# Optimization experiments

Measured on AMD Instinct MI355X. Metric: run time of the kernel, lower is better.

## Reference

```python
import jax, jax.numpy as jnp
import numpy as np

F_DIM = 512
N_HEADS = 8
D_Q = 64
D_V = 64
EPS = 1e-6


def _xavier(key, shape):
    fan_in, fan_out = shape[0], shape[1]
    limit = float(np.sqrt(6.0 / (fan_in + fan_out)))
    return jax.random.uniform(key, shape, jnp.float32, -limit, limit)


def layer_norm(x, g, b):
    mu = jnp.mean(x, axis=-1, keepdims=True)
    var = jnp.mean(jnp.square(x - mu), axis=-1, keepdims=True)
    return (x - mu) * jax.lax.rsqrt(var + EPS) * g + b


def setup_inputs() -> dict:
    key = jax.random.key(0)
    ks = jax.random.split(key, 16)
    B, V, F = 4, 2048, F_DIM
    inp = {
        "texture_map1": jax.random.normal(ks[0], (B, V, F), jnp.float32),
        "texture_map2": jax.random.normal(ks[1], (B, V, F), jnp.float32),
        "ln1_g": jnp.ones((F,), jnp.float32), "ln1_b": jnp.zeros((F,), jnp.float32),
        "ln2_g": jnp.ones((F,), jnp.float32), "ln2_b": jnp.zeros((F,), jnp.float32),
        "Wq": _xavier(ks[2], (F, N_HEADS * D_Q)), "bq": jnp.zeros((N_HEADS * D_Q,), jnp.float32),
        "Wk": _xavier(ks[3], (F, N_HEADS * D_Q)), "bk": jnp.zeros((N_HEADS * D_Q,), jnp.float32),
        "Wv": _xavier(ks[4], (F, N_HEADS * D_V)), "bv": jnp.zeros((N_HEADS * D_V,), jnp.float32),
        "Wfc": _xavier(ks[5], (N_HEADS * D_V, F)), "bfc": jnp.zeros((F,), jnp.float32),
        "ff1_ln_g": jnp.ones((F,), jnp.float32), "ff1_ln_b": jnp.zeros((F,), jnp.float32),
        "ff1_W1": _xavier(ks[6], (F, F)), "ff1_b1": jnp.zeros((F,), jnp.float32),
        "ff1_W2": _xavier(ks[7], (F, F)), "ff1_b2": jnp.zeros((F,), jnp.float32),
        "ff2_ln_g": jnp.ones((F,), jnp.float32), "ff2_ln_b": jnp.zeros((F,), jnp.float32),
        "ff2_W1": _xavier(ks[8], (F, F)), "ff2_b1": jnp.zeros((F,), jnp.float32),
        "ff2_W2": _xavier(ks[9], (F, F)), "ff2_b2": jnp.zeros((F,), jnp.float32),
    }
    return inp


def _heads(x, d):
    B, V, _ = x.shape
    return x.reshape(B, V, N_HEADS, d).transpose(0, 2, 1, 3)  # [B,H,V,d]


def _ff_block(x, ln_g, ln_b, W1, b1, W2, b2):
    h = layer_norm(x, ln_g, ln_b)
    h = jax.nn.relu(h @ W1 + b1) @ W2 + b2
    return x + h


def reference(texture_map1, texture_map2, ln1_g, ln1_b, ln2_g, ln2_b,
              Wq, bq, Wk, bk, Wv, bv, Wfc, bfc,
              ff1_ln_g, ff1_ln_b, ff1_W1, ff1_b1, ff1_W2, ff1_b2,
              ff2_ln_g, ff2_ln_b, ff2_W1, ff2_b1, ff2_W2, ff2_b2):
    B, V, F = texture_map1.shape
    norm = D_Q ** 0.5
    t1n = layer_norm(texture_map1, ln1_g, ln1_b)
    t2n = layer_norm(texture_map2, ln2_g, ln2_b)
    q1 = _heads(t1n @ Wq + bq, D_Q)
    k1 = _heads(t1n @ Wk + bk, D_Q)
    v1 = _heads(t1n @ Wv + bv, D_V)
    q2 = _heads(t2n @ Wq + bq, D_Q)
    k2 = _heads(t2n @ Wk + bk, D_Q)
    v2 = _heads(t2n @ Wv + bv, D_V)
    # cross attention: 1 attends to 2, 2 attends to 1
    attn12 = jax.nn.softmax(jnp.einsum('bhqd,bhkd->bhqk', q1, k2) / norm, axis=-1)
    attn21 = jax.nn.softmax(jnp.einsum('bhqd,bhkd->bhqk', q2, k1) / norm, axis=-1)
    f12 = jnp.einsum('bhqk,bhkd->bhqd', attn12, v2).transpose(0, 2, 1, 3).reshape(B, V, -1)
    f21 = jnp.einsum('bhqk,bhkd->bhqd', attn21, v1).transpose(0, 2, 1, 3).reshape(B, V, -1)
    f12 = f12 @ Wfc + bfc
    f21 = f21 @ Wfc + bfc
    out1 = _ff_block(texture_map1 + f12, ff1_ln_g, ff1_ln_b, ff1_W1, ff1_b1, ff1_W2, ff1_b2)
    out2 = _ff_block(texture_map2 + f21, ff2_ln_g, ff2_ln_b, ff2_W1, ff2_b1, ff2_W2, ff2_b2)
    return (out1, out2)
```

## Files before the change

### kernel.cpp

```cpp
#include <hip/hip_runtime.h>
#include <stdint.h>

#define FD    512
#define SEQ   2048
#define NHALF 8192
#define NTOT  16384
#define QKVN  1536

typedef unsigned short u16;
typedef __attribute__((ext_vector_type(8))) short short8;
typedef __attribute__((ext_vector_type(4))) float f32x4;

__device__ __forceinline__ u16 f2bf(float f){
  union { float f; uint32_t i; } v; v.f = f;
  uint32_t r = v.i + 0x7FFFu + ((v.i >> 16) & 1u);
  return (u16)(r >> 16);
}

__device__ __forceinline__ void gload_lds16(const void* g, void* l){
  __builtin_amdgcn_global_load_lds((const __attribute__((address_space(1))) void*)g,
                                   (__attribute__((address_space(3))) void*)l, 16, 0, 0);
}

__device__ __forceinline__ f32x4 mfma16(short8 a, short8 b, f32x4 c){
  return __builtin_amdgcn_mfma_f32_16x16x32_bf16(a, b, c, 0, 0, 0);
}

__device__ __forceinline__ uint32_t cvtpk(float lo, float hi){
  uint32_t r; asm("v_cvt_pk_bf16_f32 %0, %1, %2" : "=v"(r) : "v"(lo), "v"(hi)); return r;
}

__device__ __forceinline__ float fexp2(float x){
  float r; asm("v_exp_f32 %0, %1" : "=v"(r) : "v"(x)); return r;
}

__global__ __launch_bounds__(256) void wconv_kernel(
    const float* __restrict__ w0, const float* __restrict__ w1,
    const float* __restrict__ w2, const float* __restrict__ w3,
    const float* __restrict__ w4, const float* __restrict__ w5,
    const float* __restrict__ w6, const float* __restrict__ w7,
    u16* __restrict__ out)
{
  int mat = blockIdx.x >> 6;
  const float* w = w0;
  switch (mat){ case 1: w=w1; break; case 2: w=w2; break; case 3: w=w3; break;
                case 4: w=w4; break; case 5: w=w5; break; case 6: w=w6; break;
                case 7: w=w7; break; default: break; }
  int tile = blockIdx.x & 63;
  int k0 = (tile >> 3) << 6, n0 = (tile & 7) << 6;

  __shared__ float lt[64][65];
  int tid = threadIdx.x;
  int tr = tid >> 4, tc = (tid & 15) << 2;
  #pragma unroll
  for (int p = 0; p < 4; p++){
    int k = p * 16 + tr;
    float4 v = *(const float4*)&w[(size_t)(k0 + k) * 512 + n0 + tc];
    lt[k][tc] = v.x; lt[k][tc + 1] = v.y; lt[k][tc + 2] = v.z; lt[k][tc + 3] = v.w;
  }
  __syncthreads();
  int n = tid >> 2, kc = (tid & 3) << 4;
  u16 buf[16];
  #pragma unroll
  for (int j = 0; j < 16; j++) buf[j] = f2bf(lt[kc + j][n]);
  u16* dst = out + ((size_t)mat << 18) + (size_t)(n0 + n) * 512 + k0 + kc;
  *(short8*)dst       = *(const short8*)(buf);
  *(short8*)(dst + 8) = *(const short8*)(buf + 8);
}

__global__ __launch_bounds__(256) void biascat_kernel(
    const float* __restrict__ bq, const float* __restrict__ bk,
    const float* __restrict__ bv, float* __restrict__ o)
{
  int i = blockIdx.x * 256 + threadIdx.x;
  if (i < 512) o[i] = bq[i];
  else if (i < 1024) o[i] = bk[i - 512];
  else o[i] = bv[i - 1024];
}

__global__ __launch_bounds__(256) void ln_kernel(
    const float* __restrict__ xa, const float* __restrict__ xb,
    const float* __restrict__ ga, const float* __restrict__ ba,
    const float* __restrict__ gb, const float* __restrict__ bb,
    u16* __restrict__ out)
{
  int row = blockIdx.x;
  const float* x; const float* g; const float* bi;
  if (row < NHALF){ x = xa + (size_t)row * FD; g = ga; bi = ba; }
  else            { x = xb + (size_t)(row - NHALF) * FD; g = gb; bi = bb; }
  int t = threadIdx.x;
  float2 v = ((const float2*)x)[t];
  __shared__ float red[8];
  float s = v.x + v.y;
  #pragma unroll
  for (int o = 32; o; o >>= 1) s += __shfl_xor(s, o, 64);
  if ((t & 63) == 0) red[t >> 6] = s;
  __syncthreads();
  float mu = (red[0] + red[1] + red[2] + red[3]) * (1.0f / 512.0f);
  float d0 = v.x - mu, d1 = v.y - mu;
  float q = d0 * d0 + d1 * d1;
  #pragma unroll
  for (int o = 32; o; o >>= 1) q += __shfl_xor(q, o, 64);
  if ((t & 63) == 0) red[4 + (t >> 6)] = q;
  __syncthreads();
  float var = (red[4] + red[5] + red[6] + red[7]) * (1.0f / 512.0f);
  float rs = rsqrtf(var + 1e-6f);
  out[(size_t)row * FD + 2 * t]     = f2bf(d0 * rs * g[2 * t]     + bi[2 * t]);
  out[(size_t)row * FD + 2 * t + 1] = f2bf(d1 * rs * g[2 * t + 1] + bi[2 * t + 1]);
}

__global__ __launch_bounds__(256) void vtr_kernel(
    const u16* __restrict__ qkv, u16* __restrict__ vt)
{
  int kc = blockIdx.x & 15;
  int s  = blockIdx.x >> 4;
  int dir = s >> 5, b = (s >> 3) & 3, h = s & 7;
  int t = threadIdx.x;
  int d = t & 63, kb = t >> 6;
  const u16* src = qkv + (size_t)(dir * NHALF + b * SEQ + kc * 128 + kb * 32) * QKVN
                       + 1024 + h * 64 + d;
  u16* dst = vt + (size_t)s * 131072 + (size_t)d * 2048 + kc * 128 + kb * 32;
  u16 buf[32];
  #pragma unroll
  for (int j = 0; j < 32; j++) buf[j] = src[(size_t)j * QKVN];
  #pragma unroll
  for (int j = 0; j < 4; j++)
    *(short8*)(dst + j * 8) = *(const short8*)(buf + j * 8);
}

template<bool RELU, bool OUT_BF16, bool HAS_RES>
__global__ __launch_bounds__(256) void gemm_bt(
    const u16* __restrict__ A,
    const u16* __restrict__ BtLo, const u16* __restrict__ BtHi,
    const float* __restrict__ biasLo, const float* __restrict__ biasHi,
    const float* __restrict__ resLo, const float* __restrict__ resHi,
    void* __restrict__ outp,
    int M, int N, int K, int halfM)
{
  __shared__ __align__(16) u16 lA[2][128 * 32];
  __shared__ __align__(16) u16 lB[2][128 * 32];
  int nwg = gridDim.x;
  int bid = (blockIdx.x & 7) * (nwg >> 3) + (blockIdx.x >> 3);
  int nTN = N >> 7;
  int bm = bid / nTN, bn = bid - bm * nTN;
  int rowBase = bm << 7, colBase = bn << 7;
  bool lo = rowBase < halfM;
  const u16* Bt = lo ? BtLo : BtHi;
  const float* bias = lo ? biasLo : biasHi;
  const float* res = lo ? resLo : resHi;
  int rowLocalBase = lo ? rowBase : rowBase - halfM;

  int tid = threadIdx.x, wv = tid >> 6, ln = tid & 63;

  f32x4 acc[4][4];
  #pragma unroll
  for (int m = 0; m < 4; m++)
    #pragma unroll
    for (int n = 0; n < 4; n++) acc[m][n] = (f32x4){0.f, 0.f, 0.f, 0.f};

  int off0 = tid * 16, off1 = 4096 + tid * 16;
  int r0 = off0 >> 6, c0 = (off0 & 63) >> 1;
  int r1 = off1 >> 6, c1 = (off1 & 63) >> 1;
  const u16* gA0 = A + (size_t)(rowBase + r0) * K + c0;
  const u16* gA1 = A + (size_t)(rowBase + r1) * K + c1;
  const u16* gB0 = Bt + (size_t)(colBase + r0) * K + c0;
  const u16* gB1 = Bt + (size_t)(colBase + r1) * K + c1;

  int arow = (wv >> 1) << 6, bcol = (wv & 1) << 6;

  #define STAGE(buf, kt) do { \
    gload_lds16(gA0 + (kt), (char*)lA[buf] + wv * 1024); \
    gload_lds16(gA1 + (kt), (char*)lA[buf] + 4096 + wv * 1024); \
    gload_lds16(gB0 + (kt), (char*)lB[buf] + wv * 1024); \
    gload_lds16(gB1 + (kt), (char*)lB[buf] + 4096 + wv * 1024); } while (0)

  STAGE(0, 0);
  __syncthreads();

  int nK = K >> 5;
  for (int i = 0; i < nK; i++){
    int cur = i & 1;
    if (i + 1 < nK) STAGE(cur ^ 1, (i + 1) << 5);
    short8 af[4], bfr[4];
    #pragma unroll
    for (int m = 0; m < 4; m++)
      af[m] = *(const short8*)&lA[cur][(arow + (m << 4) + (ln & 15)) * 32 + ((ln >> 4) << 3)];
    #pragma unroll
    for (int n = 0; n < 4; n++)
      bfr[n] = *(const short8*)&lB[cur][(bcol + (n << 4) + (ln & 15)) * 32 + ((ln >> 4) << 3)];
    #pragma unroll
    for (int m = 0; m < 4; m++)
      #pragma unroll
      for (int n = 0; n < 4; n++)
        acc[m][n] = mfma16(af[m], bfr[n], acc[m][n]);
    __syncthreads();
  }
  #undef STAGE

  #pragma unroll
  for (int n = 0; n < 4; n++){
    int col = colBase + bcol + (n << 4) + (ln & 15);
    float bv = bias[col];
    #pragma unroll
    for (int m = 0; m < 4; m++){
      int rowT = arow + (m << 4) + ((ln >> 4) << 2);
      #pragma unroll
      for (int r = 0; r < 4; r++){
        float v = acc[m][n][r] + bv;
        if (RELU) v = fmaxf(v, 0.f);
        if (HAS_RES) v += res[(size_t)(rowLocalBase + rowT + r) * N + col];
        if (OUT_BF16) ((u16*)outp)[(size_t)(rowBase + rowT + r) * N + col] = f2bf(v);
        else ((float*)outp)[(size_t)(rowBase + rowT + r) * N + col] = v;
      }
    }
  }
}

__global__ __launch_bounds__(512, 4) void attn_kernel(
    const u16* __restrict__ qkv, const u16* __restrict__ vt, u16* __restrict__ fb)
{
  int l = (blockIdx.x & 7) * 64 + (blockIdx.x >> 3);
  int qt = l & 7;
  int h  = (l >> 3) & 7;
  int z  = l >> 6;
  int dir = z >> 2, b = z & 3;
  int qRow0  = dir * NHALF + b * SEQ + qt * 256;
  int kvRow0 = (dir ^ 1) * NHALF + b * SEQ;
  int colQ = h * 64;

  __shared__ __align__(16) u16 lK[2][64 * 64];
  __shared__ __align__(16) u16 lVt[2][64 * 64];
  __shared__ __align__(16) u16 lP[8][32 * 64];

  int tid = threadIdx.x, wv = tid >> 6, ln = tid & 63;
  int g = ln >> 4, lo = ln & 15;

  int srow = tid >> 3;
  int soff = ((tid & 7) ^ (srow & 7)) * 8;

  const float CEXP = 0.18033688f;

  int ca0 = (g * 8) ^ ((lo & 7) << 3);
  int ca1 = (32 + g * 8) ^ ((lo & 7) << 3);
  int lo64 = lo * 64;

  int pidx[4];
  #pragma unroll
  for (int n = 0; n < 4; n++)
    pidx[n] = lo64 + ((n * 16 + g * 4) ^ ((lo & 7) << 3));
  int pra = lo64 + ca0, prb = lo64 + ca1;

  const u16* qbase  = qkv + (size_t)qRow0 * QKVN + colQ;
  const u16* vtbase = vt + (size_t)((dir ^ 1) * 32 + b * 8 + h) * 131072;

  const u16* kp0 = qkv + (size_t)(kvRow0 + srow) * QKVN + 512 + colQ + soff;
  const u16* vp0 = vtbase + (size_t)srow * 2048 + soff;

  char* dK0 = (char*)lK[0] + wv * 1024;
  char* dV0 = (char*)lVt[0] + wv * 1024;
  const u16* lKf = &lK[0][0];
  const u16* lVf = &lVt[0][0];
  u16* lPw = &lP[wv][0];

  gload_lds16(qbase + (size_t)srow * QKVN + soff,         (char*)lK[0]  + wv * 1024);
  gload_lds16(qbase + (size_t)(64 + srow) * QKVN + soff,  (char*)lK[1]  + wv * 1024);
  gload_lds16(qbase + (size_t)(128 + srow) * QKVN + soff, (char*)lVt[0] + wv * 1024);
  gload_lds16(qbase + (size_t)(192 + srow) * QKVN + soff, (char*)lVt[1] + wv * 1024);
  __syncthreads();
  const u16* qh;
  switch (wv >> 1){ case 0: qh = lK[0]; break; case 1: qh = lK[1]; break;
                    case 2: qh = lVt[0]; break; default: qh = lVt[1]; break; }
  int qr0 = (wv & 1) * 32 + lo;
  short8 qf00 = *(const short8*)&qh[qr0 * 64 + ca0];
  short8 qf01 = *(const short8*)&qh[qr0 * 64 + ca1];
  short8 qf10 = *(const short8*)&qh[(qr0 + 16) * 64 + ca0];
  short8 qf11 = *(const short8*)&qh[(qr0 + 16) * 64 + ca1];
  __syncthreads();

  gload_lds16(kp0, dK0);
  gload_lds16(vp0, dV0);
  kp0 += (size_t)64 * QKVN; vp0 += 64;
  __syncthreads();

  f32x4 acc_o0[4], acc_o1[4];
  #pragma unroll
  for (int nd = 0; nd < 4; nd++){
    acc_o0[nd] = (f32x4){0.f, 0.f, 0.f, 0.f};
    acc_o1[nd] = (f32x4){0.f, 0.f, 0.f, 0.f};
  }
  f32x4 acc_l0 = (f32x4){0.f, 0.f, 0.f, 0.f};
  f32x4 acc_l1 = (f32x4){0.f, 0.f, 0.f, 0.f};
  float m_l0, m_l1;
  const f32x4 z4 = (f32x4){0.f, 0.f, 0.f, 0.f};

  short8 ones;
  #pragma unroll
  for (int j = 0; j < 8; j++) ones[j] = (short)0x3F80;

  int cb = 0;
  for (int t = 0; t < 32; t++){
    if (t < 31){
      int nb = cb ^ 8192;
      gload_lds16(kp0, dK0 + nb);
      gload_lds16(vp0, dV0 + nb);
      kp0 += (size_t)64 * QKVN; vp0 += 64;
    }
    const u16* lk = (const u16*)((const char*)lKf + cb);
    const u16* lv = (const u16*)((const char*)lVf + cb);

    f32x4 s0[4], s1[4];
    #pragma unroll
    for (int n = 0; n < 4; n++){
      short8 kfa = *(const short8*)&lk[lo64 + n * 1024 + ca0];
      short8 kfb = *(const short8*)&lk[lo64 + n * 1024 + ca1];
      s0[n] = mfma16(kfa, qf00, z4);
      s0[n] = mfma16(kfb, qf01, s0[n]);
      s1[n] = mfma16(kfa, qf10, z4);
      s1[n] = mfma16(kfb, qf11, s1[n]);
    }

    float m00, m01;
    {
      float t0 = fmaxf(fmaxf(s0[0][0], s0[0][1]), fmaxf(s0[0][2], s0[0][3]));
      float t1 = fmaxf(fmaxf(s0[1][0], s0[1][1]), fmaxf(s0[1][2], s0[1][3]));
      float t2 = fmaxf(fmaxf(s0[2][0], s0[2][1]), fmaxf(s0[2][2], s0[2][3]));
      float t3 = fmaxf(fmaxf(s0[3][0], s0[3][1]), fmaxf(s0[3][2], s0[3][3]));
      m00 = fmaxf(fmaxf(t0, t1), fmaxf(t2, t3));
      m00 = fmaxf(m00, __shfl_xor(m00, 16, 64));
      m00 = fmaxf(m00, __shfl_xor(m00, 32, 64));
      m00 *= CEXP;
    }
    {
      float t0 = fmaxf(fmaxf(s1[0][0], s1[0][1]), fmaxf(s1[0][2], s1[0][3]));
      float t1 = fmaxf(fmaxf(s1[1][0], s1[1][1]), fmaxf(s1[1][2], s1[1][3]));
      float t2 = fmaxf(fmaxf(s1[2][0], s1[2][1]), fmaxf(s1[2][2], s1[2][3]));
      float t3 = fmaxf(fmaxf(s1[3][0], s1[3][1]), fmaxf(s1[3][2], s1[3][3]));
      m01 = fmaxf(fmaxf(t0, t1), fmaxf(t2, t3));
      m01 = fmaxf(m01, __shfl_xor(m01, 16, 64));
      m01 = fmaxf(m01, __shfl_xor(m01, 32, 64));
      m01 *= CEXP;
    }

    if (t == 0){ m_l0 = m00; m_l1 = m01; }

    #pragma unroll
    for (int n = 0; n < 4; n++){
      float p0 = fexp2(fmaf(s0[n][0], CEXP, -m_l0));
      float p1 = fexp2(fmaf(s0[n][1], CEXP, -m_l0));
      float p2 = fexp2(fmaf(s0[n][2], CEXP, -m_l0));
      float p3 = fexp2(fmaf(s0[n][3], CEXP, -m_l0));
      uint2 pk0; pk0.x = cvtpk(p0, p1); pk0.y = cvtpk(p2, p3);
      *(uint2*)&lPw[pidx[n]] = pk0;
      float q0 = fexp2(fmaf(s1[n][0], CEXP, -m_l1));
      float q1 = fexp2(fmaf(s1[n][1], CEXP, -m_l1));
      float q2 = fexp2(fmaf(s1[n][2], CEXP, -m_l1));
      float q3 = fexp2(fmaf(s1[n][3], CEXP, -m_l1));
      uint2 pk1; pk1.x = cvtpk(q0, q1); pk1.y = cvtpk(q2, q3);
      *(uint2*)&lPw[pidx[n] + 1024] = pk1;
    }

    short8 pf00 = *(const short8*)&lPw[pra];
    short8 pf01 = *(const short8*)&lPw[prb];
    short8 pf10 = *(const short8*)&lPw[pra + 1024];
    short8 pf11 = *(const short8*)&lPw[prb + 1024];
    acc_l0 = mfma16(pf00, ones, acc_l0);
    acc_l0 = mfma16(pf01, ones, acc_l0);
    acc_l1 = mfma16(pf10, ones, acc_l1);
    acc_l1 = mfma16(pf11, ones, acc_l1);
    #pragma unroll
    for (int nd = 0; nd < 4; nd++){
      short8 vfa = *(const short8*)&lv[lo64 + nd * 1024 + ca0];
      short8 vfb = *(const short8*)&lv[lo64 + nd * 1024 + ca1];
      acc_o0[nd] = mfma16(pf00, vfa, acc_o0[nd]);
      acc_o0[nd] = mfma16(pf01, vfb, acc_o0[nd]);
      acc_o1[nd] = mfma16(pf10, vfa, acc_o1[nd]);
      acc_o1[nd] = mfma16(pf11, vfb, acc_o1[nd]);
    }

    bool ok = (m00 <= m_l0 + 8.f) && (m01 <= m_l1 + 8.f);
    if (!__all(ok)){
      float mn0 = fmaxf(m_l0, m00);
      float mn1 = fmaxf(m_l1, m01);
      float a00 = fexp2(m_l0 - mn0);
      float a01 = fexp2(m_l1 - mn1);
      m_l0 = mn0; m_l1 = mn1;
      #pragma unroll
      for (int r = 0; r < 4; r++){
        float ar0 = __shfl(a00, g * 4 + r, 64);
        float ar1 = __shfl(a01, g * 4 + r, 64);
        acc_l0[r] *= ar0;
        acc_l1[r] *= ar1;
        #pragma unroll
        for (int nd = 0; nd < 4; nd++){
          acc_o0[nd][r] *= ar0;
          acc_o1[nd][r] *= ar1;
        }
      }
    }

    cb ^= 8192;
    __syncthreads();
  }

  #pragma unroll
  for (int r = 0; r < 4; r++){
    float rl0 = 1.0f / acc_l0[r];
    float rl1 = 1.0f / acc_l1[r];
    #pragma unroll
    for (int nd = 0; nd < 4; nd++){
      int row0 = qRow0 + wv * 32 + g * 4 + r;
      int d    = colQ + (nd << 4) + lo;
      fb[(size_t)row0 * FD + d]        = f2bf(acc_o0[nd][r] * rl0);
      fb[(size_t)(row0 + 16) * FD + d] = f2bf(acc_o1[nd][r] * rl1);
    }
  }
}

extern "C" void kernel_launch(void* const* d_in, const int* in_sizes, int n_in,
                              void* d_out, int out_size, void* d_ws, size_t ws_size,
                              hipStream_t stream)
{
  const float* t1   = (const float*)d_in[0];
  const float* t2   = (const float*)d_in[1];
  const float* ln1g = (const float*)d_in[2];
  const float* ln1b = (const float*)d_in[3];
  const float* ln2g = (const float*)d_in[4];
  const float* ln2b = (const float*)d_in[5];
  const float* Wq   = (const float*)d_in[6];
  const float* bq   = (const float*)d_in[7];
  const float* Wk   = (const float*)d_in[8];
  const float* bk   = (const float*)d_in[9];
  const float* Wv   = (const float*)d_in[10];
  const float* bv   = (const float*)d_in[11];
  const float* Wfc  = (const float*)d_in[12];
  const float* bfc  = (const float*)d_in[13];
  const float* f1lg = (const float*)d_in[14];
  const float* f1lb = (const float*)d_in[15];
  const float* W11  = (const float*)d_in[16];
  const float* b11  = (const float*)d_in[17];
  const float* W12  = (const float*)d_in[18];
  const float* b12  = (const float*)d_in[19];
  const float* f2lg = (const float*)d_in[20];
  const float* f2lb = (const float*)d_in[21];
  const float* W21  = (const float*)d_in[22];
  const float* b21  = (const float*)d_in[23];
  const float* W22  = (const float*)d_in[24];
  const float* b22  = (const float*)d_in[25];

  char* ws = (char*)d_ws;
  const size_t MB = 1024 * 1024;
  u16* wt     = (u16*)ws;
  u16* tln    = (u16*)(ws + 4 * MB);
  u16* qkv    = (u16*)(ws + 20 * MB);
  u16* fb     = (u16*)(ws + 68 * MB);
  float* bqkv = (float*)(ws + 84 * MB);
  u16* vtb    = tln;
  u16* xln    = tln;
  u16* hb     = qkv;
  float* out  = (float*)d_out;

  wconv_kernel<<<512, 256, 0, stream>>>(Wq, Wk, Wv, Wfc, W11, W12, W21, W22, wt);
  biascat_kernel<<<6, 256, 0, stream>>>(bq, bk, bv, bqkv);
  ln_kernel<<<NTOT, 256, 0, stream>>>(t1, t2, ln1g, ln1b, ln2g, ln2b, tln);
  gemm_bt<false, true, false><<<1536, 256, 0, stream>>>(
      tln, wt, wt, bqkv, bqkv, nullptr, nullptr, qkv, NTOT, QKVN, FD, NTOT);
  vtr_kernel<<<1024, 256, 0, stream>>>(qkv, vtb);
  attn_kernel<<<512, 512, 0, stream>>>(qkv, vtb, fb);
  gemm_bt<false, false, true><<<512, 256, 0, stream>>>(
      fb, wt + 3 * 262144, wt + 3 * 262144, bfc, bfc, t1, t2, out, NTOT, FD, FD, NHALF);
  ln_kernel<<<NTOT, 256, 0, stream>>>(out, out + (size_t)NHALF * FD, f1lg, f1lb, f2lg, f2lb, xln);
  gemm_bt<true, true, false><<<512, 256, 0, stream>>>(
      xln, wt + 4 * 262144, wt + 6 * 262144, b11, b21, nullptr, nullptr, hb, NTOT, FD, FD, NHALF);
  gemm_bt<false, false, true><<<512, 256, 0, stream>>>(
      hb, wt + 5 * 262144, wt + 7 * 262144, b12, b22, out, out + (size_t)NHALF * FD, out, NTOT, FD, FD, NHALF);
}
```

Before: 235.3 us.

## Load V fragments directly from global memory into registers, drop V LDS buffer

The attention kernel no longer stages the transposed V tile through a double-buffered LDS array. Each wave now reads its V MFMA operands straight from global memory (likely served from L2, since all waves read the same tile), and issues those loads early to hide latency. The Q tile is staged in the P scratch buffer instead, so LDS use per block drops and occupancy may rise. The cost is redundant global/L2 traffic, with every wave fetching the same V data, and the PV MFMAs now wait on global load latency.

```diff
diff --git a/kernel.cpp b/kernel.cpp
--- a/kernel.cpp
+++ b/kernel.cpp
@@ -229,7 +229,6 @@
   int colQ = h * 64;
 
   __shared__ __align__(16) u16 lK[2][64 * 64];
-  __shared__ __align__(16) u16 lVt[2][64 * 64];
   __shared__ __align__(16) u16 lP[8][32 * 64];
 
   int tid = threadIdx.x, wv = tid >> 6, ln = tid & 63;
@@ -254,32 +253,27 @@
   const u16* vtbase = vt + (size_t)((dir ^ 1) * 32 + b * 8 + h) * 131072;
 
   const u16* kp0 = qkv + (size_t)(kvRow0 + srow) * QKVN + 512 + colQ + soff;
-  const u16* vp0 = vtbase + (size_t)srow * 2048 + soff;
+  const u16* vg = vtbase + (size_t)lo * 2048 + g * 8;
 
   char* dK0 = (char*)lK[0] + wv * 1024;
-  char* dV0 = (char*)lVt[0] + wv * 1024;
   const u16* lKf = &lK[0][0];
-  const u16* lVf = &lVt[0][0];
+  u16* lPf = &lP[0][0];
   u16* lPw = &lP[wv][0];
 
-  gload_lds16(qbase + (size_t)srow * QKVN + soff,         (char*)lK[0]  + wv * 1024);
-  gload_lds16(qbase + (size_t)(64 + srow) * QKVN + soff,  (char*)lK[1]  + wv * 1024);
-  gload_lds16(qbase + (size_t)(128 + srow) * QKVN + soff, (char*)lVt[0] + wv * 1024);
-  gload_lds16(qbase + (size_t)(192 + srow) * QKVN + soff, (char*)lVt[1] + wv * 1024);
-  __syncthreads();
-  const u16* qh;
-  switch (wv >> 1){ case 0: qh = lK[0]; break; case 1: qh = lK[1]; break;
-                    case 2: qh = lVt[0]; break; default: qh = lVt[1]; break; }
-  int qr0 = (wv & 1) * 32 + lo;
-  short8 qf00 = *(const short8*)&qh[qr0 * 64 + ca0];
-  short8 qf01 = *(const short8*)&qh[qr0 * 64 + ca1];
-  short8 qf10 = *(const short8*)&qh[(qr0 + 16) * 64 + ca0];
-  short8 qf11 = *(const short8*)&qh[(qr0 + 16) * 64 + ca1];
+  gload_lds16(qbase + (size_t)srow * QKVN + soff,         (char*)lPf + wv * 1024);
+  gload_lds16(qbase + (size_t)(64 + srow) * QKVN + soff,  (char*)lPf + 8192 + wv * 1024);
+  gload_lds16(qbase + (size_t)(128 + srow) * QKVN + soff, (char*)lPf + 16384 + wv * 1024);
+  gload_lds16(qbase + (size_t)(192 + srow) * QKVN + soff, (char*)lPf + 24576 + wv * 1024);
+  __syncthreads();
+  int qr = wv * 32 + lo;
+  short8 qf00 = *(const short8*)&lPf[qr * 64 + ca0];
+  short8 qf01 = *(const short8*)&lPf[qr * 64 + ca1];
+  short8 qf10 = *(const short8*)&lPf[(qr + 16) * 64 + ca0];
+  short8 qf11 = *(const short8*)&lPf[(qr + 16) * 64 + ca1];
   __syncthreads();
 
   gload_lds16(kp0, dK0);
-  gload_lds16(vp0, dV0);
-  kp0 += (size_t)64 * QKVN; vp0 += 64;
+  kp0 += (size_t)64 * QKVN;
   __syncthreads();
 
   f32x4 acc_o0[4], acc_o1[4];
@@ -300,13 +294,16 @@
   int cb = 0;
   for (int t = 0; t < 32; t++){
     if (t < 31){
-      int nb = cb ^ 8192;
-      gload_lds16(kp0, dK0 + nb);
-      gload_lds16(vp0, dV0 + nb);
-      kp0 += (size_t)64 * QKVN; vp0 += 64;
+      gload_lds16(kp0, dK0 + (cb ^ 8192));
+      kp0 += (size_t)64 * QKVN;
     }
     const u16* lk = (const u16*)((const char*)lKf + cb);
-    const u16* lv = (const u16*)((const char*)lVf + cb);
+
+    const u16* vrow = vg + (t << 6);
+    short8 va0 = *(const short8*)(vrow);
+    short8 va1 = *(const short8*)(vrow + 16 * 2048);
+    short8 va2 = *(const short8*)(vrow + 32 * 2048);
+    short8 va3 = *(const short8*)(vrow + 48 * 2048);
 
     f32x4 s0[4], s1[4];
     #pragma unroll
@@ -359,6 +356,11 @@
       *(uint2*)&lPw[pidx[n] + 1024] = pk1;
     }
 
+    short8 vb0 = *(const short8*)(vrow + 32);
+    short8 vb1 = *(const short8*)(vrow + 16 * 2048 + 32);
+    short8 vb2 = *(const short8*)(vrow + 32 * 2048 + 32);
+    short8 vb3 = *(const short8*)(vrow + 48 * 2048 + 32);
+
     short8 pf00 = *(const short8*)&lPw[pra];
     short8 pf01 = *(const short8*)&lPw[prb];
     short8 pf10 = *(const short8*)&lPw[pra + 1024];
@@ -367,15 +369,22 @@
     acc_l0 = mfma16(pf01, ones, acc_l0);
     acc_l1 = mfma16(pf10, ones, acc_l1);
     acc_l1 = mfma16(pf11, ones, acc_l1);
-    #pragma unroll
-    for (int nd = 0; nd < 4; nd++){
-      short8 vfa = *(const short8*)&lv[lo64 + nd * 1024 + ca0];
-      short8 vfb = *(const short8*)&lv[lo64 + nd * 1024 + ca1];
-      acc_o0[nd] = mfma16(pf00, vfa, acc_o0[nd]);
-      acc_o0[nd] = mfma16(pf01, vfb, acc_o0[nd]);
-      acc_o1[nd] = mfma16(pf10, vfa, acc_o1[nd]);
-      acc_o1[nd] = mfma16(pf11, vfb, acc_o1[nd]);
-    }
+    acc_o0[0] = mfma16(pf00, va0, acc_o0[0]);
+    acc_o0[0] = mfma16(pf01, vb0, acc_o0[0]);
+    acc_o1[0] = mfma16(pf10, va0, acc_o1[0]);
+    acc_o1[0] = mfma16(pf11, vb0, acc_o1[0]);
+    acc_o0[1] = mfma16(pf00, va1, acc_o0[1]);
+    acc_o0[1] = mfma16(pf01, vb1, acc_o0[1]);
+    acc_o1[1] = mfma16(pf10, va1, acc_o1[1]);
+    acc_o1[1] = mfma16(pf11, vb1, acc_o1[1]);
+    acc_o0[2] = mfma16(pf00, va2, acc_o0[2]);
+    acc_o0[2] = mfma16(pf01, vb2, acc_o0[2]);
+    acc_o1[2] = mfma16(pf10, va2, acc_o1[2]);
+    acc_o1[2] = mfma16(pf11, vb2, acc_o1[2]);
+    acc_o0[3] = mfma16(pf00, va3, acc_o0[3]);
+    acc_o0[3] = mfma16(pf01, vb3, acc_o0[3]);
+    acc_o1[3] = mfma16(pf10, va3, acc_o1[3]);
+    acc_o1[3] = mfma16(pf11, vb3, acc_o1[3]);
 
     bool ok = (m00 <= m_l0 + 8.f) && (m01 <= m_l1 + 8.f);
     if (!__all(ok)){
```

New measurement: 273.8 us. 1.16x slower.
